# Kernel tuning notes

Measured on AMD Instinct MI355X. Metric: run time of the kernel, lower is better.

## Reference

```python
import jax, jax.numpy as jnp
import numpy as np
import math

DIM = 1024
NH = 16
HD = DIM // NH
SEQ = 2048
B = 2
P = 16
HIDDEN = 2816  # multiple_of*ceil(int(2*4*dim/3)/multiple_of)


def justnorm(x, axis=-1):
    n = jnp.sqrt(jnp.sum(x * x, axis=axis, keepdims=True))
    return x / jnp.maximum(n, 1e-12)


def adafm_modulate(x, ftime, p):
    # x: [B,H,W]; ftime: [B, p*p] real
    Bb, H, W = x.shape
    xp = x.reshape(Bb, H // p, p, W // p, p).transpose(0, 1, 3, 2, 4).reshape(Bb, H // p, W // p, p * p)
    fspec = jnp.fft.fft2(xp)  # over last two axes (W//p, p*p)
    fspec = fspec * ftime.reshape(Bb, 1, 1, p * p)
    fout = jnp.fft.ifft2(fspec).real
    fout = fout.reshape(Bb, H // p, W // p, p, p).transpose(0, 1, 3, 2, 4).reshape(Bb, H, W)
    return fout


def apply_rotary(xq, xk, cos, sin):
    # xq,xk: [B,S,NH,HD]; cos,sin: [S, HD//2]
    def rot(t):
        tr = t.reshape(*t.shape[:-1], HD // 2, 2)
        a, b = tr[..., 0], tr[..., 1]
        c = cos[None, :, None, :]
        s = sin[None, :, None, :]
        ra = a * c - b * s
        rb = a * s + b * c
        return jnp.stack([ra, rb], axis=-1).reshape(t.shape)
    return rot(xq), rot(xk)


def attention(x, cos, sin, wq, wk, wv, wo, sqk):
    bsz, seqlen, _ = x.shape
    xq = (x @ wq).reshape(bsz, seqlen, NH, HD)
    xk = (x @ wk).reshape(bsz, seqlen, NH, HD)
    xv = (x @ wv).reshape(bsz, seqlen, NH, HD)
    xq, xk = apply_rotary(xq, xk, cos, sin)
    sqk_eff = (sqk * math.sqrt(DIM)).reshape(1, 1, NH, HD)  # sqk_init_value/sqk_init_scaling = sqrt(dim)
    xq = sqk_eff * justnorm(xq)
    xk = sqk_eff * justnorm(xk)
    scale = HD ** 0.5
    scores = jnp.einsum('bqhd,bkhd->bhqk', xq, xk) * scale
    attn = jax.nn.softmax(scores, axis=-1)
    out = jnp.einsum('bhqk,bkhd->bqhd', attn, xv).reshape(bsz, seqlen, DIM)
    return out @ wo


def feed_forward(x, w1, w2, w3, su, sv):
    x1 = x @ w1
    x3 = x @ w3
    scale = math.sqrt(HIDDEN)
    h = jax.nn.silu(x1 * sv * scale) * (x3 * su)
    return h @ w2


def setup_inputs() -> dict:
    key = jax.random.key(0)
    ks = jax.random.split(key, 12)
    inv = 1.0 / (10000.0 ** (np.arange(0, HD, 2, dtype=np.float32) / HD))
    ang = np.outer(np.arange(SEQ, dtype=np.float32), inv)
    s = 0.02
    return {
        'x': jax.random.normal(ks[0], (B, SEQ, DIM), jnp.float32),
        'freqs_cos': jnp.asarray(np.cos(ang), jnp.float32),
        'freqs_sin': jnp.asarray(np.sin(ang), jnp.float32),
        'adafm_input': jax.random.normal(ks[1], (B, DIM), jnp.float32),
        'wq': jax.random.normal(ks[2], (DIM, DIM), jnp.float32) * s,
        'wk': jax.random.normal(ks[3], (DIM, DIM), jnp.float32) * s,
        'wv': jax.random.normal(ks[4], (DIM, DIM), jnp.float32) * s,
        'wo': jax.random.normal(ks[5], (DIM, DIM), jnp.float32) * s,
        'sqk': jnp.full((DIM,), 1.0 / math.sqrt(DIM), jnp.float32),
        'w1': jax.random.normal(ks[6], (DIM, HIDDEN), jnp.float32) * s,
        'w2': jax.random.normal(ks[7], (HIDDEN, DIM), jnp.float32) * s,
        'w3': jax.random.normal(ks[8], (DIM, HIDDEN), jnp.float32) * s,
        'su': jnp.ones((HIDDEN,), jnp.float32),
        'sv': jnp.ones((HIDDEN,), jnp.float32),
        'proj_w': jax.random.normal(ks[9], (DIM, 2 * P * P), jnp.float32) * s,
        'proj_b': jnp.zeros((2 * P * P,), jnp.float32),
        'attn_alpha': jnp.full((DIM,), 0.05 / math.sqrt(DIM), jnp.float32),
        'mlp_alpha': jnp.full((DIM,), 0.05 / math.sqrt(DIM), jnp.float32),
    }


def reference(x, freqs_cos, freqs_sin, adafm_input, wq, wk, wv, wo, sqk, w1, w2, w3, su, sv, proj_w, proj_b, attn_alpha, mlp_alpha):
    # AdaFM projection: SiLU -> Linear
    t = jax.nn.silu(adafm_input) @ proj_w + proj_b  # [B, 2*P*P]
    msa_time, mlp_time = t[:, :P * P], t[:, P * P:]

    alpha_scale = 0.05 * math.sqrt(DIM)  # attn_alpha_init_value / attn_alpha_init_scaling
    lr = jnp.abs(attn_alpha * alpha_scale)
    h = justnorm(x)
    h_a = attention(adafm_modulate(x, msa_time, P), freqs_cos, freqs_sin, wq, wk, wv, wo, sqk)
    h_a = justnorm(h_a)
    x = justnorm(h + lr * (h_a - h))

    lr = jnp.abs(mlp_alpha * alpha_scale)
    h = justnorm(x)
    h_m = feed_forward(adafm_modulate(x, mlp_time, P), w1, w2, w3, su, sv)
    h_m = justnorm(h_m)
    x = justnorm(h + lr * (h_m - h))
    return x
```

## Files before the change

### kernel.cpp

```cpp
#include <hip/hip_runtime.h>
#include <hip/hip_bf16.h>
#include <math.h>

#define SEQ    2048
#define DIMN   1024
#define NHEAD  16
#define HDIM   64
#define BATCH  2
#define ROWS   4096
#define HIDDEN 2816
#define FCHUNK 2048
#define QKVS   3072

typedef __attribute__((ext_vector_type(8))) short short8;
typedef __attribute__((ext_vector_type(4))) float f32x4;
typedef unsigned short ushort_t;
typedef __attribute__((address_space(1))) void gas_t;
typedef __attribute__((address_space(3))) void las_t;

__device__ __forceinline__ float bfbits(ushort_t u){ return __uint_as_float(((unsigned)u) << 16); }
__device__ __forceinline__ ushort_t f2bu(float f){
  __hip_bfloat16 h = __float2bfloat16(f);
  return *reinterpret_cast<ushort_t*>(&h);
}
__device__ __forceinline__ ushort_t f2bu_t(float f){ return (ushort_t)(__float_as_uint(f) >> 16); }
__device__ __forceinline__ float ldv(const float* p){ return *p; }
__device__ __forceinline__ float ldv(const ushort_t* p){ return bfbits(*p); }
__device__ __forceinline__ void stv(float* p, float v){ *p = v; }
__device__ __forceinline__ void stv(ushort_t* p, float v){ *p = f2bu(v); }
__device__ __forceinline__ void async_cp16(const ushort_t* g, ushort_t* l){
  __builtin_amdgcn_global_load_lds((gas_t*)g, (las_t*)l, 16, 0, 0);
}
__device__ __forceinline__ ushort4 ld4u(const float* p){
  float4 v = *(const float4*)p;
  ushort4 u; u.x = f2bu(v.x); u.y = f2bu(v.y); u.z = f2bu(v.z); u.w = f2bu(v.w);
  return u;
}
__device__ __forceinline__ ushort4 ld4u(const ushort_t* p){ return *(const ushort4*)p; }

__global__ void k_time(const float* __restrict__ ada, const float* __restrict__ pw,
                       const float* __restrict__ pb, float* __restrict__ t){
  int b = blockIdx.x >> 9, o = blockIdx.x & 511, lane = threadIdx.x;
  float acc = 0.f;
  for(int i = lane; i < DIMN; i += 64){
    float a = ada[b*DIMN + i];
    float s = a / (1.f + expf(-a));
    acc += s * pw[i*512 + o];
  }
  for(int off = 32; off; off >>= 1) acc += __shfl_down(acc, off);
  if(lane == 0) t[b*512 + o] = acc + pb[o];
}

__global__ void k_gp(const float* __restrict__ t, ushort_t* __restrict__ Gpk){
  __shared__ float gl[256];
  int wb = blockIdx.x, kc = blockIdx.y, tid = threadIdx.x;
  int b = wb & 1, which = wb >> 1;
  const float C = 6.283185307179586f / 256.f;
  float acc = 0.f;
  for(int k = 0; k < 256; k++){
    float f = t[b*512 + which*256 + k];
    acc += f * cosf(C * (float)((k*tid) & 255));
  }
  gl[tid] = acc * (1.f/256.f);
  __syncthreads();
  ushort_t* ob = Gpk + ((size_t)(wb*8 + kc))*8192;
  for(int rep = 0; rep < 4; rep++){
    int n = rep*64 + (tid >> 2), mmb = (tid & 3)*8;
    short8 o;
    #pragma unroll
    for(int j = 0; j < 8; j++)
      o[j] = (short)f2bu(gl[(n - kc*32 - (mmb + j)) & 255]);
    *(short8*)(ob + n*32 + mmb) = o;
  }
}

#define APAD 264
#define GPAD 40
template<typename IN>
__global__ __launch_bounds__(256) void k_modmf(const IN* __restrict__ src,
        const ushort_t* __restrict__ Gpk, ushort_t* __restrict__ dst){
  __shared__ __align__(16) ushort_t Ap[64*APAD];
  __shared__ __align__(16) ushort_t Gs[128*GPAD];
  int nh = blockIdx.x, i = blockIdx.y, b = blockIdx.z;
  int tid = threadIdx.x, lane = tid & 63, w = tid >> 6;
  int l15 = lane & 15, quad = lane >> 4;
  const IN* xb = src + (size_t)b*SEQ*DIMN + (size_t)(i*16)*DIMN;
  int j = tid >> 2, c = (tid & 3)*4;
  #pragma unroll 4
  for(int rep = 0; rep < 16; rep++){
    ushort4 v4 = ld4u(xb + (size_t)rep*DIMN + tid*4);
    *(ushort4*)&Ap[j*APAD + rep*16 + c] = v4;
  }
  f32x4 acc[8];
  #pragma unroll
  for(int nt = 0; nt < 8; nt++){ acc[nt][0]=0.f; acc[nt][1]=0.f; acc[nt][2]=0.f; acc[nt][3]=0.f; }
  for(int kc = 0; kc < 8; kc++){
    __syncthreads();
    {
      const ushort_t* gsrc = Gpk + ((size_t)(b*8 + kc))*8192 + nh*4096;
      #pragma unroll
      for(int r2 = 0; r2 < 2; r2++){
        int n = r2*64 + (tid >> 2), mm = (tid & 3)*8;
        *(short8*)&Gs[n*GPAD + mm] = *(const short8*)(gsrc + r2*2048 + tid*8);
      }
    }
    __syncthreads();
    short8 af = *(const short8*)&Ap[(w*16 + l15)*APAD + kc*32 + quad*8];
    #pragma unroll
    for(int nt = 0; nt < 8; nt++){
      short8 bf = *(const short8*)&Gs[(nt*16 + l15)*GPAD + quad*8];
      acc[nt] = __builtin_amdgcn_mfma_f32_16x16x32_bf16(af, bf, acc[nt], 0, 0, 0);
    }
  }
  size_t ob = (size_t)b*SEQ*DIMN + (size_t)(i*16 + nh*8)*DIMN + (w*16 + quad*4)*16 + l15;
  #pragma unroll
  for(int nt = 0; nt < 8; nt++)
    #pragma unroll
    for(int t = 0; t < 4; t++)
      dst[ob + (size_t)nt*DIMN + t*16] = f2bu(acc[nt][t]);
}

__global__ void k_wt(const float* __restrict__ W, ushort_t* __restrict__ Wt, int K, int N){
  __shared__ float tile[32][33];
  int k0 = blockIdx.y*32, n0 = blockIdx.x*32;
  int r = threadIdx.x >> 3, c4 = (threadIdx.x & 7)*4;
  float4 v = *(const float4*)(W + (size_t)(k0 + r)*N + n0 + c4);
  tile[r][c4+0] = v.x; tile[r][c4+1] = v.y; tile[r][c4+2] = v.z; tile[r][c4+3] = v.w;
  __syncthreads();
  ushort4 o;
  o.x = f2bu(tile[c4+0][r]); o.y = f2bu(tile[c4+1][r]);
  o.z = f2bu(tile[c4+2][r]); o.w = f2bu(tile[c4+3][r]);
  *(ushort4*)(Wt + (size_t)(n0 + r)*K + k0 + c4) = o;
}

template<int BM, int BN, typename OUT>
__global__ __launch_bounds__(256) void k_gemm_mf(const ushort_t* __restrict__ A,
        const ushort_t* __restrict__ Wt, OUT* __restrict__ C, int N, int K){
  constexpr int MT = BM/32, NT = BN/32;
  constexpr int AI = BM/64, BI = BN/64;
  __shared__ __align__(16) ushort_t As[BM*32];
  __shared__ __align__(16) ushort_t Bs[BN*32];
  int tid = threadIdx.x, lane = tid & 63, w = tid >> 6;
  int l15 = lane & 15, quad = lane >> 4;
  int m0 = blockIdx.y*BM, n0 = blockIdx.x*BN;
  int wr = (w>>1)*(BM/2), wc = (w&1)*(BN/2);
  int srow = lane >> 2, scol = (lane & 3)*8;
  const ushort_t* ag[AI]; ushort_t* al[AI];
  const ushort_t* bg[BI]; ushort_t* bl[BI];
  #pragma unroll
  for(int i = 0; i < AI; i++){
    int rb = w*AI + i;
    ag[i] = A + (size_t)(m0 + rb*16 + srow)*K + scol;
    al[i] = As + rb*512 + lane*8;
  }
  #pragma unroll
  for(int i = 0; i < BI; i++){
    int rb = w*BI + i;
    bg[i] = Wt + (size_t)(n0 + rb*16 + srow)*K + scol;
    bl[i] = Bs + rb*512 + lane*8;
  }
  f32x4 acc[MT][NT];
  #pragma unroll
  for(int mt = 0; mt < MT; mt++)
    #pragma unroll
    for(int nt = 0; nt < NT; nt++)
      for(int t = 0; t < 4; t++) acc[mt][nt][t] = 0.f;
  for(int kk = 0; kk < K; kk += 32){
    __syncthreads();
    #pragma unroll
    for(int i = 0; i < AI; i++) async_cp16(ag[i] + kk, al[i]);
    #pragma unroll
    for(int i = 0; i < BI; i++) async_cp16(bg[i] + kk, bl[i]);
    __syncthreads();
    short8 af[MT], bf[NT];
    #pragma unroll
    for(int mt = 0; mt < MT; mt++) af[mt] = *(const short8*)&As[(wr + mt*16 + l15)*32 + quad*8];
    #pragma unroll
    for(int nt = 0; nt < NT; nt++) bf[nt] = *(const short8*)&Bs[(wc + nt*16 + l15)*32 + quad*8];
    #pragma unroll
    for(int mt = 0; mt < MT; mt++)
      #pragma unroll
      for(int nt = 0; nt < NT; nt++)
        acc[mt][nt] = __builtin_amdgcn_mfma_f32_16x16x32_bf16(af[mt], bf[nt], acc[mt][nt], 0, 0, 0);
  }
  #pragma unroll
  for(int mt = 0; mt < MT; mt++)
    #pragma unroll
    for(int nt = 0; nt < NT; nt++)
      #pragma unroll
      for(int t = 0; t < 4; t++)
        stv(C + (size_t)(m0 + wr + mt*16 + quad*4 + t)*N + n0 + wc + nt*16 + l15, acc[mt][nt][t]);
}

__global__ __launch_bounds__(256) void k_ffn12(const ushort_t* __restrict__ A,
        const ushort_t* __restrict__ W1t, const ushort_t* __restrict__ W3t,
        const float* __restrict__ su, const float* __restrict__ sv,
        ushort_t* __restrict__ H, int K){
  __shared__ __align__(16) ushort_t As[128*32];
  __shared__ __align__(16) ushort_t B1s[64*32];
  __shared__ __align__(16) ushort_t B3s[64*32];
  int tid = threadIdx.x, lane = tid & 63, w = tid >> 6;
  int l15 = lane & 15, quad = lane >> 4;
  int m0 = blockIdx.y*128, n0 = blockIdx.x*64;
  int wr = (w>>1)*64, wc = (w&1)*32;
  int srow = lane >> 2, scol = (lane & 3)*8;
  const ushort_t* ag[2]; ushort_t* al[2];
  #pragma unroll
  for(int i = 0; i < 2; i++){
    int rb = w*2 + i;
    ag[i] = A + (size_t)(m0 + rb*16 + srow)*K + scol;
    al[i] = As + rb*512 + lane*8;
  }
  const ushort_t* b1g = W1t + (size_t)(n0 + w*16 + srow)*K + scol;
  const ushort_t* b3g = W3t + (size_t)(n0 + w*16 + srow)*K + scol;
  ushort_t* b1l = B1s + w*512 + lane*8;
  ushort_t* b3l = B3s + w*512 + lane*8;
  f32x4 acc1[4][2], acc3[4][2];
  #pragma unroll
  for(int mt = 0; mt < 4; mt++)
    #pragma unroll
    for(int nt = 0; nt < 2; nt++)
      for(int t = 0; t < 4; t++){ acc1[mt][nt][t] = 0.f; acc3[mt][nt][t] = 0.f; }
  for(int kk = 0; kk < K; kk += 32){
    __syncthreads();
    async_cp16(ag[0] + kk, al[0]);
    async_cp16(ag[1] + kk, al[1]);
    async_cp16(b1g + kk, b1l);
    async_cp16(b3g + kk, b3l);
    __syncthreads();
    short8 af[4], b1f[2], b3f[2];
    #pragma unroll
    for(int mt = 0; mt < 4; mt++) af[mt] = *(const short8*)&As[(wr + mt*16 + l15)*32 + quad*8];
    #pragma unroll
    for(int nt = 0; nt < 2; nt++){
      b1f[nt] = *(const short8*)&B1s[(wc + nt*16 + l15)*32 + quad*8];
      b3f[nt] = *(const short8*)&B3s[(wc + nt*16 + l15)*32 + quad*8];
    }
    #pragma unroll
    for(int mt = 0; mt < 4; mt++)
      #pragma unroll
      for(int nt = 0; nt < 2; nt++){
        acc1[mt][nt] = __builtin_amdgcn_mfma_f32_16x16x32_bf16(af[mt], b1f[nt], acc1[mt][nt], 0, 0, 0);
        acc3[mt][nt] = __builtin_amdgcn_mfma_f32_16x16x32_bf16(af[mt], b3f[nt], acc3[mt][nt], 0, 0, 0);
      }
  }
  #pragma unroll
  for(int nt = 0; nt < 2; nt++){
    int n = n0 + wc + nt*16 + l15;
    float svv = sv[n] * 53.06599665f, suv = su[n];
    #pragma unroll
    for(int mt = 0; mt < 4; mt++)
      #pragma unroll
      for(int t = 0; t < 4; t++){
        float hpre = acc1[mt][nt][t] * svv;
        float sil = hpre / (1.f + expf(-hpre));
        float hv = sil * (acc3[mt][nt][t] * suv);
        H[(size_t)(m0 + wr + mt*16 + quad*4 + t)*HIDDEN + n] = f2bu(hv);
      }
  }
}

__global__ void k_qkvprep(ushort_t* __restrict__ qkv, const float* __restrict__ fc,
        const float* __restrict__ fs, const float* __restrict__ sqk){
  int w = threadIdx.x >> 6, d = threadIdx.x & 63;
  int h = blockIdx.x*4 + w, s = blockIdx.y, b = blockIdx.z;
  size_t ib = ((size_t)(b*SEQ + s))*QKVS + h*HDIM + d;
  float q = bfbits(qkv[ib]), k = bfbits(qkv[ib + 1024]);
  float qn = __shfl_xor(q, 1), kn = __shfl_xor(k, 1);
  int p = d >> 1;
  float c = fc[s*32 + p], sn = fs[s*32 + p];
  float qr, kr;
  if((d & 1) == 0){ qr = q*c - qn*sn; kr = k*c - kn*sn; }
  else            { qr = qn*sn + q*c; kr = kn*sn + k*c; }
  float sq = qr*qr, sk = kr*kr;
  for(int off = 32; off; off >>= 1){ sq += __shfl_xor(sq, off); sk += __shfl_xor(sk, off); }
  float scl = sqk[h*HDIM + d] * 32.f;
  qkv[ib]        = f2bu(scl * qr / fmaxf(sqrtf(sq), 1e-12f));
  qkv[ib + 1024] = f2bu(scl * kr / fmaxf(sqrtf(sk), 1e-12f));
}

__global__ void k_vt(const ushort_t* __restrict__ qkv, ushort_t* __restrict__ vto){
  __shared__ ushort_t tile[64][72];
  int s0 = blockIdx.x*64, h = blockIdx.y, b = blockIdx.z;
  int r = threadIdx.x >> 2, c = (threadIdx.x & 3)*16;
  const ushort_t* src = qkv + (size_t)(b*SEQ + s0 + r)*QKVS + 2048 + h*HDIM + c;
  *(short8*)&tile[r][c]     = *(const short8*)src;
  *(short8*)&tile[r][c + 8] = *(const short8*)(src + 8);
  __syncthreads();
  ushort_t* dst = vto + ((size_t)(b*NHEAD + h)*HDIM + r)*SEQ + s0 + c;
  for(int j = 0; j < 16; j += 4){
    ushort4 o;
    o.x = tile[c+j][r]; o.y = tile[c+j+1][r]; o.z = tile[c+j+2][r]; o.w = tile[c+j+3][r];
    *(ushort4*)(dst + j) = o;
  }
}

#define LSTR 72
__global__ __launch_bounds__(256) void k_flash_mf(const ushort_t* __restrict__ qkv,
        const ushort_t* __restrict__ vt, ushort_t* __restrict__ out){
  int qb = blockIdx.x, h = blockIdx.y, b = blockIdx.z;
  int tid = threadIdx.x, lane = tid & 63, w = tid >> 6;
  int l15 = lane & 15, quad = lane >> 4;
  __shared__ __align__(16) ushort_t Ks[64*LSTR], Vts[64*LSTR];
  __shared__ __align__(16) ushort_t Ps[4][16*LSTR];
  size_t qkb = (size_t)b*SEQ*QKVS + h*HDIM;
  size_t ob  = (size_t)b*SEQ*DIMN + h*HDIM;
  const ushort_t* vb = vt + (size_t)(b*NHEAD + h)*HDIM*SEQ;
  short8 qf0, qf1;
  {
    const ushort_t* qrow = qkv + qkb + (size_t)(qb*64 + w*16 + l15)*QKVS;
    qf0 = *(const short8*)(qrow + quad*8);
    qf1 = *(const short8*)(qrow + 32 + quad*8);
  }
  f32x4 o_acc[4];
  #pragma unroll
  for(int g = 0; g < 4; g++){ o_acc[g][0]=0.f; o_acc[g][1]=0.f; o_acc[g][2]=0.f; o_acc[g][3]=0.f; }
  float lsum = 0.f;
  int sr = tid >> 2, sc = tid & 3;
  const ushort_t* kbase = qkv + qkb + 1024 + (size_t)sr*QKVS + sc*16;
  const ushort_t* vbase = vb + (size_t)sr*SEQ + sc*16;
  short8 kr0 = *(const short8*)kbase,       kr1 = *(const short8*)(kbase + 8);
  short8 vr0 = *(const short8*)vbase,       vr1 = *(const short8*)(vbase + 8);
  const float C1 = 11.54156036f;
  const float C2 = 11.90223409f;
  for(int ch = 0; ch < SEQ/64; ch++){
    __syncthreads();
    *(short8*)&Ks[sr*LSTR + sc*16]      = kr0;
    *(short8*)&Ks[sr*LSTR + sc*16 + 8]  = kr1;
    *(short8*)&Vts[sr*LSTR + sc*16]     = vr0;
    *(short8*)&Vts[sr*LSTR + sc*16 + 8] = vr1;
    if(ch + 1 < SEQ/64){
      const ushort_t* kn = kbase + (size_t)(ch + 1)*64*QKVS;
      const ushort_t* vn = vbase + (ch + 1)*64;
      kr0 = *(const short8*)kn; kr1 = *(const short8*)(kn + 8);
      vr0 = *(const short8*)vn; vr1 = *(const short8*)(vn + 8);
    }
    __syncthreads();
    #pragma unroll
    for(int g = 0; g < 4; g++){
      f32x4 sa; sa[0]=0.f; sa[1]=0.f; sa[2]=0.f; sa[3]=0.f;
      short8 k0 = *(const short8*)&Ks[(g*16 + l15)*LSTR + quad*8];
      short8 k1 = *(const short8*)&Ks[(g*16 + l15)*LSTR + 32 + quad*8];
      sa = __builtin_amdgcn_mfma_f32_16x16x32_bf16(k0, qf0, sa, 0, 0, 0);
      sa = __builtin_amdgcn_mfma_f32_16x16x32_bf16(k1, qf1, sa, 0, 0, 0);
      float e0 = exp2f(fmaf(sa[0], C1, -C2));
      float e1 = exp2f(fmaf(sa[1], C1, -C2));
      float e2 = exp2f(fmaf(sa[2], C1, -C2));
      float e3 = exp2f(fmaf(sa[3], C1, -C2));
      lsum += (e0 + e1) + (e2 + e3);
      ushort4 pk;
      pk.x = f2bu_t(e0); pk.y = f2bu_t(e1); pk.z = f2bu_t(e2); pk.w = f2bu_t(e3);
      *(ushort4*)&Ps[w][l15*LSTR + g*16 + quad*4] = pk;
    }
    short8 a0 = *(const short8*)&Ps[w][l15*LSTR + quad*8];
    short8 a1 = *(const short8*)&Ps[w][l15*LSTR + 32 + quad*8];
    #pragma unroll
    for(int g = 0; g < 4; g++){
      short8 b0 = *(const short8*)&Vts[(g*16 + l15)*LSTR + quad*8];
      short8 b1 = *(const short8*)&Vts[(g*16 + l15)*LSTR + 32 + quad*8];
      o_acc[g] = __builtin_amdgcn_mfma_f32_16x16x32_bf16(a0, b0, o_acc[g], 0, 0, 0);
      o_acc[g] = __builtin_amdgcn_mfma_f32_16x16x32_bf16(a1, b1, o_acc[g], 0, 0, 0);
    }
  }
  lsum += __shfl_xor(lsum, 16);
  lsum += __shfl_xor(lsum, 32);
  #pragma unroll
  for(int t = 0; t < 4; t++){
    float inv = 1.f / __shfl(lsum, quad*4 + t);
    #pragma unroll
    for(int g = 0; g < 4; g++)
      out[ob + (size_t)(qb*64 + w*16 + quad*4 + t)*DIMN + g*16 + l15] = f2bu(o_acc[g][t] * inv);
  }
}

__device__ __forceinline__ float blockReduceSum(float v, float* red){
  for(int off = 32; off; off >>= 1) v += __shfl_xor(v, off);
  int wid = threadIdx.x >> 6;
  if((threadIdx.x & 63) == 0) red[wid] = v;
  __syncthreads();
  float tot = red[0] + red[1] + red[2] + red[3];
  __syncthreads();
  return tot;
}

template<typename T1, typename T2, typename TO>
__global__ void k_rn(const T1* __restrict__ x, const T2* __restrict__ ha,
        const float* __restrict__ alpha, TO* __restrict__ xo){
  __shared__ float red[4];
  int row = blockIdx.x, tid = threadIdx.x;
  size_t base = (size_t)row * DIMN;
  float xs[4], hs[4], cs[4];
  float s1 = 0.f, s2 = 0.f;
  for(int j = 0; j < 4; j++){
    int i = tid + j*256;
    float xv = ldv(x + base + i);  xs[j] = xv; s1 += xv*xv;
    float hv = ldv(ha + base + i); hs[j] = hv; s2 += hv*hv;
  }
  s1 = blockReduceSum(s1, red);
  s2 = blockReduceSum(s2, red);
  float r1 = 1.f / fmaxf(sqrtf(s1), 1e-12f);
  float r2 = 1.f / fmaxf(sqrtf(s2), 1e-12f);
  float s3 = 0.f;
  for(int j = 0; j < 4; j++){
    int i = tid + j*256;
    float lr = fabsf(alpha[i] * 1.6f);
    float hn = xs[j] * r1;
    float cv = hn + lr*(hs[j]*r2 - hn);
    cs[j] = cv; s3 += cv*cv;
  }
  s3 = blockReduceSum(s3, red);
  float r3 = 1.f / fmaxf(sqrtf(s3), 1e-12f);
  for(int j = 0; j < 4; j++){
    int i = tid + j*256;
    stv(xo + base + i, cs[j] * r3);
  }
}

extern "C" void kernel_launch(void* const* d_in, const int* in_sizes, int n_in,
                              void* d_out, int out_size, void* d_ws, size_t ws_size,
                              hipStream_t stream){
  const float* x   = (const float*)d_in[0];
  const float* fc  = (const float*)d_in[1];
  const float* fs  = (const float*)d_in[2];
  const float* ada = (const float*)d_in[3];
  const float* wq  = (const float*)d_in[4];
  const float* wk  = (const float*)d_in[5];
  const float* wv  = (const float*)d_in[6];
  const float* wo  = (const float*)d_in[7];
  const float* sqk = (const float*)d_in[8];
  const float* w1  = (const float*)d_in[9];
  const float* w2  = (const float*)d_in[10];
  const float* w3  = (const float*)d_in[11];
  const float* su  = (const float*)d_in[12];
  const float* sv  = (const float*)d_in[13];
  const float* pw  = (const float*)d_in[14];
  const float* pb  = (const float*)d_in[15];
  const float* aal = (const float*)d_in[16];
  const float* mal = (const float*)d_in[17];
  float* out = (float*)d_out;

  const size_t MM = (size_t)DIMN*DIMN;
  const size_t HM = (size_t)HIDDEN*DIMN;
  const size_t F  = (size_t)ROWS*DIMN;
  char* wsb = (char*)d_ws;
  float* t = (float*)wsb;
  ushort_t* Gpk = (ushort_t*)(wsb + 16384);
  ushort_t* wqT = Gpk + 262144;
  ushort_t* wkT = wqT + MM;
  ushort_t* wvT = wkT + MM;
  ushort_t* woT = wvT + MM;
  ushort_t* w1T = woT + MM;
  ushort_t* w3T = w1T + HM;
  ushort_t* w2T = w3T + HM;
  ushort_t* P1  = w2T + HM;
  ushort_t* QKV = P1 + F;
  ushort_t* Ha  = QKV;
  ushort_t* M2  = QKV + F;
  ushort_t* Hm  = QKV + 2*F;
  ushort_t* a1  = QKV + 3*F;
  ushort_t* Vt  = a1;

  dim3 blk(256);

  k_time<<<dim3(1024), dim3(64), 0, stream>>>(ada, pw, pb, t);
  k_gp<<<dim3(4,8), blk, 0, stream>>>(t, Gpk);

  k_wt<<<dim3(32,32), blk, 0, stream>>>(wq, wqT, DIMN, DIMN);
  k_wt<<<dim3(32,32), blk, 0, stream>>>(wk, wkT, DIMN, DIMN);
  k_wt<<<dim3(32,32), blk, 0, stream>>>(wv, wvT, DIMN, DIMN);
  k_wt<<<dim3(32,32), blk, 0, stream>>>(wo, woT, DIMN, DIMN);
  k_wt<<<dim3(HIDDEN/32,32), blk, 0, stream>>>(w1, w1T, DIMN, HIDDEN);
  k_wt<<<dim3(HIDDEN/32,32), blk, 0, stream>>>(w3, w3T, DIMN, HIDDEN);
  k_wt<<<dim3(32,HIDDEN/32), blk, 0, stream>>>(w2, w2T, HIDDEN, DIMN);

  k_modmf<float><<<dim3(2,128,BATCH), blk, 0, stream>>>(x, Gpk, P1);
  k_gemm_mf<128,128,ushort_t><<<dim3(24,32), blk, 0, stream>>>(P1, wqT, QKV, QKVS, DIMN);
  k_qkvprep<<<dim3(NHEAD/4,SEQ,BATCH), blk, 0, stream>>>(QKV, fc, fs, sqk);
  k_vt<<<dim3(SEQ/64,NHEAD,BATCH), blk, 0, stream>>>(QKV, Vt);
  k_flash_mf<<<dim3(SEQ/64,NHEAD,BATCH), blk, 0, stream>>>(QKV, Vt, P1);
  k_gemm_mf<128,64,ushort_t><<<dim3(16,32), blk, 0, stream>>>(P1, woT, Ha, DIMN, DIMN);
  k_rn<float,ushort_t,ushort_t><<<dim3(ROWS), blk, 0, stream>>>(x, Ha, aal, P1);

  k_modmf<ushort_t><<<dim3(2,128,BATCH), blk, 0, stream>>>(P1, Gpk + 131072, M2);
  for(int c2 = 0; c2 < ROWS/FCHUNK; c2++){
    const ushort_t* Ac = M2 + (size_t)c2*FCHUNK*DIMN;
    k_ffn12<<<dim3(HIDDEN/64,FCHUNK/128), blk, 0, stream>>>(Ac, w1T, w3T, su, sv, a1, DIMN);
    k_gemm_mf<64,64,ushort_t><<<dim3(16,FCHUNK/64), blk, 0, stream>>>(a1, w2T, Hm + (size_t)c2*FCHUNK*DIMN, DIMN, HIDDEN);
  }

  k_rn<ushort_t,ushort_t,float><<<dim3(ROWS), blk, 0, stream>>>(P1, Hm, mal, out);
}
```

Measured before the change: 512.4 us.

## Batch weight transposes, fuse QKV prep with V transpose, unchunk FFN

The seven per-weight transpose launches are merged into one launch. Each block finds its job from a table of start offsets. The RoPE and normalisation kernel for Q/K is fused with the V-transpose kernel, so each thread now handles 16 contiguous elements with vector loads and a 4-lane reduction. The FFN no longer runs in two row chunks: it runs once over all rows, and the w2 GEMM uses a 128x64 tile. This cuts launch count and small-kernel overhead, but the a1 intermediate now needs room for every row, which depends on workspace sizing not visible here.

```diff
diff --git a/kernel.cpp b/kernel.cpp
--- a/kernel.cpp
+++ b/kernel.cpp
@@ -9,7 +9,6 @@
 #define BATCH  2
 #define ROWS   4096
 #define HIDDEN 2816
-#define FCHUNK 2048
 #define QKVS   3072
 
 typedef __attribute__((ext_vector_type(8))) short short8;
@@ -120,9 +119,19 @@
       dst[ob + (size_t)nt*DIMN + t*16] = f2bu(acc[nt][t]);
 }
 
-__global__ void k_wt(const float* __restrict__ W, ushort_t* __restrict__ Wt, int K, int N){
+struct WtJob { const float* src; ushort_t* dst; int K, N, nx, tstart; };
+struct WtJobs { WtJob j[7]; };
+__global__ __launch_bounds__(256) void k_wtall(WtJobs jobs){
   __shared__ float tile[32][33];
-  int k0 = blockIdx.y*32, n0 = blockIdx.x*32;
+  int bid = blockIdx.x;
+  int ji = 0;
+  #pragma unroll
+  for(int i = 1; i < 7; i++) if(bid >= jobs.j[i].tstart) ji = i;
+  const float* W = jobs.j[ji].src;
+  ushort_t* Wt = jobs.j[ji].dst;
+  int K = jobs.j[ji].K, N = jobs.j[ji].N;
+  int tt = bid - jobs.j[ji].tstart;
+  int n0 = (tt % jobs.j[ji].nx)*32, k0 = (tt / jobs.j[ji].nx)*32;
   int r = threadIdx.x >> 3, c4 = (threadIdx.x & 7)*4;
   float4 v = *(const float4*)(W + (size_t)(k0 + r)*N + n0 + c4);
   tile[r][c4+0] = v.x; tile[r][c4+1] = v.y; tile[r][c4+2] = v.z; tile[r][c4+3] = v.w;
@@ -260,38 +269,54 @@
   }
 }
 
-__global__ void k_qkvprep(ushort_t* __restrict__ qkv, const float* __restrict__ fc,
+__global__ __launch_bounds__(256) void k_qkvt(ushort_t* __restrict__ qkv,
+        ushort_t* __restrict__ vto, const float* __restrict__ fc,
         const float* __restrict__ fs, const float* __restrict__ sqk){
-  int w = threadIdx.x >> 6, d = threadIdx.x & 63;
-  int h = blockIdx.x*4 + w, s = blockIdx.y, b = blockIdx.z;
-  size_t ib = ((size_t)(b*SEQ + s))*QKVS + h*HDIM + d;
-  float q = bfbits(qkv[ib]), k = bfbits(qkv[ib + 1024]);
-  float qn = __shfl_xor(q, 1), kn = __shfl_xor(k, 1);
-  int p = d >> 1;
-  float c = fc[s*32 + p], sn = fs[s*32 + p];
-  float qr, kr;
-  if((d & 1) == 0){ qr = q*c - qn*sn; kr = k*c - kn*sn; }
-  else            { qr = qn*sn + q*c; kr = kn*sn + k*c; }
-  float sq = qr*qr, sk = kr*kr;
-  for(int off = 32; off; off >>= 1){ sq += __shfl_xor(sq, off); sk += __shfl_xor(sk, off); }
-  float scl = sqk[h*HDIM + d] * 32.f;
-  qkv[ib]        = f2bu(scl * qr / fmaxf(sqrtf(sq), 1e-12f));
-  qkv[ib + 1024] = f2bu(scl * kr / fmaxf(sqrtf(sk), 1e-12f));
-}
-
-__global__ void k_vt(const ushort_t* __restrict__ qkv, ushort_t* __restrict__ vto){
   __shared__ ushort_t tile[64][72];
   int s0 = blockIdx.x*64, h = blockIdx.y, b = blockIdx.z;
-  int r = threadIdx.x >> 2, c = (threadIdx.x & 3)*16;
-  const ushort_t* src = qkv + (size_t)(b*SEQ + s0 + r)*QKVS + 2048 + h*HDIM + c;
-  *(short8*)&tile[r][c]     = *(const short8*)src;
-  *(short8*)&tile[r][c + 8] = *(const short8*)(src + 8);
+  int tid = threadIdx.x;
+  int r = tid >> 2, c = (tid & 3)*16;
+  const ushort_t* vsrc = qkv + (size_t)(b*SEQ + s0 + r)*QKVS + 2048 + h*HDIM + c;
+  *(short8*)&tile[r][c]     = *(const short8*)vsrc;
+  *(short8*)&tile[r][c + 8] = *(const short8*)(vsrc + 8);
+  size_t qb_ = (size_t)(b*SEQ + s0 + r)*QKVS + h*HDIM + c;
+  short8 q0 = *(const short8*)(qkv + qb_),        q1 = *(const short8*)(qkv + qb_ + 8);
+  short8 k0 = *(const short8*)(qkv + qb_ + 1024), k1 = *(const short8*)(qkv + qb_ + 1032);
+  int s = s0 + r;
+  float qr[16], kr[16];
+  float sq = 0.f, sk = 0.f;
+  #pragma unroll
+  for(int j = 0; j < 16; j += 2){
+    float qa = bfbits((ushort_t)(j < 8 ? q0[j] : q1[j-8]));
+    float qb2 = bfbits((ushort_t)(j+1 < 8 ? q0[j+1] : q1[j-7]));
+    float ka = bfbits((ushort_t)(j < 8 ? k0[j] : k1[j-8]));
+    float kb2 = bfbits((ushort_t)(j+1 < 8 ? k0[j+1] : k1[j-7]));
+    float co = fc[s*32 + ((c + j) >> 1)], si = fs[s*32 + ((c + j) >> 1)];
+    qr[j]   = qa*co - qb2*si;  qr[j+1] = qa*si + qb2*co;
+    kr[j]   = ka*co - kb2*si;  kr[j+1] = ka*si + kb2*co;
+    sq += qr[j]*qr[j] + qr[j+1]*qr[j+1];
+    sk += kr[j]*kr[j] + kr[j+1]*kr[j+1];
+  }
+  sq += __shfl_xor(sq, 1); sq += __shfl_xor(sq, 2);
+  sk += __shfl_xor(sk, 1); sk += __shfl_xor(sk, 2);
+  float rq = 1.f / fmaxf(sqrtf(sq), 1e-12f);
+  float rk = 1.f / fmaxf(sqrtf(sk), 1e-12f);
+  short8 oq0, oq1, ok0, ok1;
+  #pragma unroll
+  for(int j = 0; j < 8; j++){
+    float s0v = sqk[h*HDIM + c + j] * 32.f;
+    float s1v = sqk[h*HDIM + c + 8 + j] * 32.f;
+    oq0[j] = (short)f2bu(s0v*qr[j]*rq);   oq1[j] = (short)f2bu(s1v*qr[8+j]*rq);
+    ok0[j] = (short)f2bu(s0v*kr[j]*rk);   ok1[j] = (short)f2bu(s1v*kr[8+j]*rk);
+  }
+  *(short8*)(qkv + qb_)        = oq0;  *(short8*)(qkv + qb_ + 8)    = oq1;
+  *(short8*)(qkv + qb_ + 1024) = ok0;  *(short8*)(qkv + qb_ + 1032) = ok1;
   __syncthreads();
   ushort_t* dst = vto + ((size_t)(b*NHEAD + h)*HDIM + r)*SEQ + s0 + c;
-  for(int j = 0; j < 16; j += 4){
+  for(int j2 = 0; j2 < 16; j2 += 4){
     ushort4 o;
-    o.x = tile[c+j][r]; o.y = tile[c+j+1][r]; o.z = tile[c+j+2][r]; o.w = tile[c+j+3][r];
-    *(ushort4*)(dst + j) = o;
+    o.x = tile[c+j2][r]; o.y = tile[c+j2+1][r]; o.z = tile[c+j2+2][r]; o.w = tile[c+j2+3][r];
+    *(ushort4*)(dst + j2) = o;
   }
 }
 
@@ -319,8 +344,8 @@
   int sr = tid >> 2, sc = tid & 3;
   const ushort_t* kbase = qkv + qkb + 1024 + (size_t)sr*QKVS + sc*16;
   const ushort_t* vbase = vb + (size_t)sr*SEQ + sc*16;
-  short8 kr0 = *(const short8*)kbase,       kr1 = *(const short8*)(kbase + 8);
-  short8 vr0 = *(const short8*)vbase,       vr1 = *(const short8*)(vbase + 8);
+  short8 kr0 = *(const short8*)kbase, kr1 = *(const short8*)(kbase + 8);
+  short8 vr0 = *(const short8*)vbase, vr1 = *(const short8*)(vbase + 8);
   const float C1 = 11.54156036f;
   const float C2 = 11.90223409f;
   for(int ch = 0; ch < SEQ/64; ch++){
@@ -465,28 +490,25 @@
   k_time<<<dim3(1024), dim3(64), 0, stream>>>(ada, pw, pb, t);
   k_gp<<<dim3(4,8), blk, 0, stream>>>(t, Gpk);
 
-  k_wt<<<dim3(32,32), blk, 0, stream>>>(wq, wqT, DIMN, DIMN);
-  k_wt<<<dim3(32,32), blk, 0, stream>>>(wk, wkT, DIMN, DIMN);
-  k_wt<<<dim3(32,32), blk, 0, stream>>>(wv, wvT, DIMN, DIMN);
-  k_wt<<<dim3(32,32), blk, 0, stream>>>(wo, woT, DIMN, DIMN);
-  k_wt<<<dim3(HIDDEN/32,32), blk, 0, stream>>>(w1, w1T, DIMN, HIDDEN);
-  k_wt<<<dim3(HIDDEN/32,32), blk, 0, stream>>>(w3, w3T, DIMN, HIDDEN);
-  k_wt<<<dim3(32,HIDDEN/32), blk, 0, stream>>>(w2, w2T, HIDDEN, DIMN);
+  WtJobs jobs;
+  jobs.j[0] = {wq, wqT, DIMN, DIMN, 32, 0};
+  jobs.j[1] = {wk, wkT, DIMN, DIMN, 32, 1024};
+  jobs.j[2] = {wv, wvT, DIMN, DIMN, 32, 2048};
+  jobs.j[3] = {wo, woT, DIMN, DIMN, 32, 3072};
+  jobs.j[4] = {w1, w1T, DIMN, HIDDEN, HIDDEN/32, 4096};
+  jobs.j[5] = {w3, w3T, DIMN, HIDDEN, HIDDEN/32, 4096 + 2816};
+  jobs.j[6] = {w2, w2T, HIDDEN, DIMN, 32, 4096 + 5632};
+  k_wtall<<<dim3(12544), blk, 0, stream>>>(jobs);
 
   k_modmf<float><<<dim3(2,128,BATCH), blk, 0, stream>>>(x, Gpk, P1);
   k_gemm_mf<128,128,ushort_t><<<dim3(24,32), blk, 0, stream>>>(P1, wqT, QKV, QKVS, DIMN);
-  k_qkvprep<<<dim3(NHEAD/4,SEQ,BATCH), blk, 0, stream>>>(QKV, fc, fs, sqk);
-  k_vt<<<dim3(SEQ/64,NHEAD,BATCH), blk, 0, stream>>>(QKV, Vt);
+  k_qkvt<<<dim3(SEQ/64,NHEAD,BATCH), blk, 0, stream>>>(QKV, Vt, fc, fs, sqk);
   k_flash_mf<<<dim3(SEQ/64,NHEAD,BATCH), blk, 0, stream>>>(QKV, Vt, P1);
   k_gemm_mf<128,64,ushort_t><<<dim3(16,32), blk, 0, stream>>>(P1, woT, Ha, DIMN, DIMN);
   k_rn<float,ushort_t,ushort_t><<<dim3(ROWS), blk, 0, stream>>>(x, Ha, aal, P1);
 
   k_modmf<ushort_t><<<dim3(2,128,BATCH), blk, 0, stream>>>(P1, Gpk + 131072, M2);
-  for(int c2 = 0; c2 < ROWS/FCHUNK; c2++){
-    const ushort_t* Ac = M2 + (size_t)c2*FCHUNK*DIMN;
-    k_ffn12<<<dim3(HIDDEN/64,FCHUNK/128), blk, 0, stream>>>(Ac, w1T, w3T, su, sv, a1, DIMN);
-    k_gemm_mf<64,64,ushort_t><<<dim3(16,FCHUNK/64), blk, 0, stream>>>(a1, w2T, Hm + (size_t)c2*FCHUNK*DIMN, DIMN, HIDDEN);
-  }
-
+  k_ffn12<<<dim3(HIDDEN/64,ROWS/128), blk, 0, stream>>>(M2, w1T, w3T, su, sv, a1, DIMN);
+  k_gemm_mf<128,64,ushort_t><<<dim3(16,32), blk, 0, stream>>>(a1, w2T, Hm, DIMN, HIDDEN);
   k_rn<ushort_t,ushort_t,float><<<dim3(ROWS), blk, 0, stream>>>(P1, Hm, mal, out);
 }
```

Measured after the change: 495.7 us. 3.3% less time.
